# Optimization experiments

Measured on AMD Instinct MI355X. Metric: run time of the kernel, lower is better.

The kernel has to match this reference:

```python
import jax, jax.numpy as jnp
import numpy as np

D_MODEL = 128
D_INNER = 256
D_STATE = 16
D_CONV = 4
DT_RANK = 8
GROUPS = 4


def setup_inputs() -> dict:
    key = jax.random.key(0)
    ks = jax.random.split(key, 8)
    x = jax.random.normal(ks[0], (2, D_MODEL, 64, 64), dtype=jnp.float32)
    Win = jax.random.normal(ks[1], (2 * D_INNER, D_MODEL), dtype=jnp.float32) * (D_MODEL ** -0.5)
    conv_w = jax.random.normal(ks[2], (D_INNER, 1, D_CONV), dtype=jnp.float32) * 0.2
    conv_b = jnp.zeros((D_INNER,), dtype=jnp.float32)
    Wx = jax.random.normal(ks[3], (DT_RANK + 2 * D_STATE, D_INNER), dtype=jnp.float32) * (D_INNER ** -0.5)
    Wdt = jax.random.normal(ks[4], (D_INNER, DT_RANK), dtype=jnp.float32) * (DT_RANK ** -0.5)
    # bias chosen so softplus(bdt) ~ 0.01 (standard mamba dt init range)
    bdt = jnp.full((D_INNER,), -4.6, dtype=jnp.float32) + 0.1 * jax.random.normal(ks[5], (D_INNER,), dtype=jnp.float32)
    A_log = jnp.log(jnp.broadcast_to(jnp.arange(1, D_STATE + 1, dtype=jnp.float32), (D_INNER, D_STATE)))
    D = jnp.ones((D_INNER,), dtype=jnp.float32)
    Wout = jax.random.normal(ks[6], (D_MODEL, D_INNER), dtype=jnp.float32) * (D_INNER ** -0.5)
    gn_w = jnp.ones((D_MODEL,), dtype=jnp.float32)
    gn_b = jnp.zeros((D_MODEL,), dtype=jnp.float32)
    return {"x": x, "Win": Win, "conv_w": conv_w, "conv_b": conv_b, "Wx": Wx,
            "Wdt": Wdt, "bdt": bdt, "A_log": A_log, "D": D, "Wout": Wout,
            "gn_w": gn_w, "gn_b": gn_b}


def _mamba(xf, Win, conv_w, conv_b, Wx, Wdt, bdt, A_log, D, Wout):
    # xf: [1, L, d_model]
    d_inner = conv_w.shape[0]
    d_state = A_log.shape[1]
    xz = jnp.einsum('blc,ec->ble', xf, Win)                # [1, L, 2*di]
    u, z = jnp.split(xz, 2, axis=-1)
    # causal depthwise conv1d (pad left d_conv-1)
    uT = jnp.swapaxes(u, 1, 2)                             # [1, di, L]
    conv = jax.lax.conv_general_dilated(
        uT, conv_w, window_strides=(1,), padding=[(D_CONV - 1, 0)],
        feature_group_count=d_inner, dimension_numbers=('NCH', 'OIH', 'NCH'))
    u = jax.nn.silu(jnp.swapaxes(conv, 1, 2) + conv_b)      # [1, L, di]
    x_dbl = jnp.einsum('bld,ed->ble', u, Wx)
    dt = x_dbl[..., :DT_RANK]
    Bm = x_dbl[..., DT_RANK:DT_RANK + d_state]              # [1, L, n]
    Cm = x_dbl[..., DT_RANK + d_state:]                     # [1, L, n]
    delta = jax.nn.softplus(jnp.einsum('blr,dr->bld', dt, Wdt) + bdt)
    A = -jnp.exp(A_log)                                     # [di, n]
    dA = jnp.exp(jnp.einsum('bld,dn->bldn', delta, A))      # [1, L, di, n]
    dBu = jnp.einsum('bld,bln,bld->bldn', delta, Bm, u)     # [1, L, di, n]

    def step(h, inp):
        dA_l, dBu_l, C_l = inp
        h = dA_l * h + dBu_l                                # [1, di, n]
        y = jnp.einsum('bdn,bn->bd', h, C_l)
        return h, y

    h0 = jnp.zeros((1, d_inner, d_state), dtype=u.dtype)
    _, ys = jax.lax.scan(step, h0,
                         (jnp.swapaxes(dA, 0, 1), jnp.swapaxes(dBu, 0, 1), jnp.swapaxes(Cm, 0, 1)))
    y = jnp.swapaxes(ys, 0, 1)                              # [1, L, di]
    y = y + u * D
    y = y * jax.nn.silu(z)
    return jnp.einsum('bld,od->blo', y, Wout)


def reference(x, Win, conv_w, conv_b, Wx, Wdt, bdt, A_log, D, Wout, gn_w, gn_b):
    B, C, H, W = x.shape
    x_flat = jnp.transpose(x, (0, 2, 3, 1)).reshape(1, -1, C)   # [1, B*H*W, C]
    args = (Win, conv_w, conv_b, Wx, Wdt, bdt, A_log, D, Wout)
    y_fwd = _mamba(x_flat, *args)
    y_bwd = jnp.flip(_mamba(jnp.flip(x_flat, axis=1), *args), axis=1)
    x_recon = (y_fwd + y_bwd).reshape(B, H, W, C)
    x_recon = jnp.transpose(x_recon, (0, 3, 1, 2))              # [B, C, H, W]
    # GroupNorm(GROUPS, C) + SiLU
    xg = x_recon.reshape(B, GROUPS, C // GROUPS, H, W)
    mu = xg.mean(axis=(2, 3, 4), keepdims=True)
    var = xg.var(axis=(2, 3, 4), keepdims=True)
    xn = ((xg - mu) * jax.lax.rsqrt(var + 1e-5)).reshape(B, C, H, W)
    xn = xn * gn_w[:, None, None] + gn_b[:, None, None]
    return jax.nn.silu(xn) + x
```

## Files before the change

### kernel.cpp

```cpp
#include <hip/hip_runtime.h>
#include <math.h>

#define L_SEQ 8192
#define TCH 16
#define NCH 512

typedef short v8s __attribute__((ext_vector_type(8)));
typedef float v4f __attribute__((ext_vector_type(4)));

__device__ __forceinline__ float silu_f(float v) { return v / (1.f + expf(-v)); }

__device__ __forceinline__ unsigned short f2bf(float f) {
    unsigned u = __float_as_uint(f);
    u += 0x7fffu + ((u >> 16) & 1u);
    return (unsigned short)(u >> 16);
}
__device__ __forceinline__ float bf2f(unsigned short s) {
    return __uint_as_float(((unsigned)s) << 16);
}

__global__ __launch_bounds__(256) void k_xz_gemm(const float* __restrict__ x,
                                                 const float* __restrict__ Win,
                                                 const float* __restrict__ Wx,
                                                 const float* __restrict__ Wout,
                                                 float* __restrict__ ubuf,
                                                 float* __restrict__ zbuf,
                                                 unsigned short* __restrict__ Wx_bf,
                                                 unsigned short* __restrict__ Wout_bf) {
    if (blockIdx.y == 8) {
        int tid = blockIdx.x * 256 + threadIdx.x;
        if (tid < 10240) Wx_bf[tid] = f2bf(Wx[tid]);
        Wout_bf[tid] = f2bf(Wout[tid]);
        return;
    }
    __shared__ __align__(16) unsigned short As[64][136];
    __shared__ __align__(16) unsigned short Bs[64][136];
    int l0 = blockIdx.x * 64;
    int e0 = blockIdx.y * 64;
    int t = threadIdx.x;
    const float* xb = x + (l0 >> 12) * (128 * 4096) + (l0 & 4095);
    #pragma unroll
    for (int i = 0; i < 16; ++i) {
        int flat = t + 256 * i;
        int ll = flat & 63, cp = flat >> 6;
        float v0 = xb[(2 * cp) * 4096 + ll];
        float v1 = xb[(2 * cp + 1) * 4096 + ll];
        unsigned pk = (unsigned)f2bf(v0) | ((unsigned)f2bf(v1) << 16);
        *(unsigned*)&As[ll][2 * cp] = pk;
    }
    #pragma unroll
    for (int i = 0; i < 16; ++i) {
        int f = t + 256 * i;
        int row = f >> 6, cp = f & 63;
        float v0 = Win[(e0 + row) * 128 + 2 * cp];
        float v1 = Win[(e0 + row) * 128 + 2 * cp + 1];
        unsigned pk = (unsigned)f2bf(v0) | ((unsigned)f2bf(v1) << 16);
        *(unsigned*)&Bs[row][2 * cp] = pk;
    }
    __syncthreads();
    int lane = t & 63, wv = t >> 6;
    int quad = lane >> 4, l16 = lane & 15;
    v4f acc[4];
    #pragma unroll
    for (int nt = 0; nt < 4; ++nt) acc[nt] = (v4f){0.f, 0.f, 0.f, 0.f};
    #pragma unroll
    for (int k0 = 0; k0 < 128; k0 += 32) {
        v8s a = *(const v8s*)&As[wv * 16 + l16][k0 + quad * 8];
        #pragma unroll
        for (int nt = 0; nt < 4; ++nt) {
            v8s b = *(const v8s*)&Bs[nt * 16 + l16][k0 + quad * 8];
            acc[nt] = __builtin_amdgcn_mfma_f32_16x16x32_bf16(a, b, acc[nt], 0, 0, 0);
        }
    }
    #pragma unroll
    for (int nt = 0; nt < 4; ++nt) {
        int e = e0 + nt * 16 + l16;
        #pragma unroll
        for (int r = 0; r < 4; ++r) {
            int l = l0 + wv * 16 + quad * 4 + r;
            float v = acc[nt][r];
            if (e < 256) ubuf[l * 256 + e] = v;
            else         zbuf[l * 256 + e - 256] = v;
        }
    }
}

__global__ __launch_bounds__(256, 4) void k_pass1(const float* __restrict__ ubuf,
                                                  const unsigned short* __restrict__ Wx_bf,
                                                  const float* __restrict__ cw,
                                                  const float* __restrict__ cb,
                                                  const float* __restrict__ Wdt,
                                                  const float* __restrict__ bdt,
                                                  const float* __restrict__ Dp,
                                                  float* __restrict__ Cc,
                                                  float* __restrict__ cumSb,
                                                  unsigned short* __restrict__ ylb,
                                                  float* __restrict__ Sb,
                                                  unsigned short* __restrict__ Qb) {
    __shared__ __align__(16) unsigned short ucst[16][264];
    __shared__ __align__(16) unsigned short wxs[48][264];
    __shared__ float xs[16][48];
    int blk = blockIdx.x;
    int dir = blk >> 9, chunk = blk & 511;
    int m0 = chunk * TCH;
    int d = threadIdx.x;
    {
        const uint4* wxb = (const uint4*)Wx_bf;
        #pragma unroll
        for (int i = 0; i < 5; ++i) {
            int f = d + 256 * i;
            int row = f >> 5, col = (f & 31) * 8;
            *(uint4*)&wxs[row][col] = wxb[f];
        }
        uint4 z4 = {0u, 0u, 0u, 0u};
        int row = 40 + (d >> 5), col = (d & 31) * 8;
        *(uint4*)&wxs[row][col] = z4;
    }
    {
        float4 w4 = *(const float4*)&cw[d * 4];
        float cbd = cb[d];
        int m = m0 - 3;
        float p3 = (m >= 0) ? ubuf[(dir ? (8191 - m) : m) * 256 + d] : 0.f;
        m = m0 - 2;
        float p2 = (m >= 0) ? ubuf[(dir ? (8191 - m) : m) * 256 + d] : 0.f;
        m = m0 - 1;
        float p1 = (m >= 0) ? ubuf[(dir ? (8191 - m) : m) * 256 + d] : 0.f;
        #pragma unroll
        for (int i = 0; i < 16; ++i) {
            int mm = m0 + i;
            int l = dir ? (8191 - mm) : mm;
            float cur = ubuf[l * 256 + d];
            float v = cbd + w4.x * p3 + w4.y * p2 + w4.z * p1 + w4.w * cur;
            ucst[i][d] = f2bf(silu_f(v));
            p3 = p2; p2 = p1; p1 = cur;
        }
    }
    __syncthreads();
    {
        int lane = d & 63, wv = d >> 6;
        int quad = lane >> 4, l16 = lane & 15;
        if (wv < 3) {
            v4f acc = {0.f, 0.f, 0.f, 0.f};
            #pragma unroll
            for (int k0 = 0; k0 < 256; k0 += 32) {
                v8s a = *(const v8s*)&ucst[l16][k0 + quad * 8];
                v8s b = *(const v8s*)&wxs[wv * 16 + l16][k0 + quad * 8];
                acc = __builtin_amdgcn_mfma_f32_16x16x32_bf16(a, b, acc, 0, 0, 0);
            }
            #pragma unroll
            for (int r = 0; r < 4; ++r)
                xs[quad * 4 + r][wv * 16 + l16] = acc[r];
        }
    }
    __syncthreads();
    int gbase = dir * L_SEQ + m0;
    {
        int tl = d >> 4, n = d & 15;
        Cc[(gbase + tl) * 16 + n] = xs[tl][24 + n];
    }
    float wdt[8];
    *(float4*)&wdt[0] = *(const float4*)&Wdt[d * 8];
    *(float4*)&wdt[4] = *(const float4*)&Wdt[d * 8 + 4];
    float bd = bdt[d], Dd = Dp[d];
    float h[16];
    #pragma unroll
    for (int n = 0; n < 16; ++n) h[n] = 0.f;
    float cumS = 0.f;
    for (int tl = 0; tl < 16; ++tl) {
        float a = bd;
        #pragma unroll
        for (int r = 0; r < 8; ++r) a = fmaf(xs[tl][r], wdt[r], a);
        float dlt = (a > 20.f) ? a : log1pf(expf(a));
        cumS += dlt;
        float rr = expf(-dlt);
        float uq = bf2f(ucst[tl][d]);
        float p = dlt * uq;
        float am = 1.f, y = 0.f;
        #pragma unroll
        for (int n = 0; n < 16; ++n) {
            am *= rr;
            h[n] = fmaf(am, h[n], p * xs[tl][8 + n]);
            y = fmaf(h[n], xs[tl][24 + n], y);
        }
        int g = gbase + tl;
        cumSb[g * 256 + d] = cumS;
        ylb[g * 256 + d] = f2bf(fmaf(uq, Dd, y));
    }
    int cbk = dir * NCH + chunk;
    Sb[cbk * 256 + d] = cumS;
    #pragma unroll
    for (int n = 0; n < 16; ++n) Qb[(cbk * 16 + n) * 256 + d] = f2bf(h[n]);
}

__global__ __launch_bounds__(256, 4) void k_scan2(const float* __restrict__ Sb,
                                                  const unsigned short* __restrict__ Qb,
                                                  unsigned short* __restrict__ Hin) {
    __shared__ float Ag[8][32], Bg[8][32];
    int blk = blockIdx.x;
    int dir = blk >> 7;
    int rem = blk & 127;
    int n = rem >> 3, dg = rem & 7;
    int t = threadIdx.x;
    int cg = t >> 5, dl = t & 31;
    int d = dg * 32 + dl;
    float np1 = (float)(n + 1);
    int cbase = dir * NCH + cg * 64;
    float A = 1.f, B = 0.f;
    #pragma unroll 4
    for (int i = 0; i < 64; ++i) {
        int cbk = cbase + i;
        float a = expf(-Sb[cbk * 256 + d] * np1);
        float b = bf2f(Qb[(cbk * 16 + n) * 256 + d]);
        A = a * A;
        B = fmaf(a, B, b);
    }
    Ag[cg][dl] = A; Bg[cg][dl] = B;
    __syncthreads();
    float H = 0.f;
    for (int g = 0; g < cg; ++g) H = fmaf(Ag[g][dl], H, Bg[g][dl]);
    #pragma unroll 4
    for (int i = 0; i < 64; ++i) {
        int cbk = cbase + i;
        Hin[(cbk * 16 + n) * 256 + d] = f2bf(H);
        float a = expf(-Sb[cbk * 256 + d] * np1);
        float b = bf2f(Qb[(cbk * 16 + n) * 256 + d]);
        H = fmaf(a, H, b);
    }
}

__global__ __launch_bounds__(512) void k_yout(const float* __restrict__ cumSb,
                                              const unsigned short* __restrict__ ylb,
                                              const float* __restrict__ Cc,
                                              const unsigned short* __restrict__ Hin,
                                              const float* __restrict__ zbuf,
                                              const unsigned short* __restrict__ Wout_bf,
                                              float* __restrict__ outp,
                                              float* __restrict__ pbuf) {
    __shared__ __align__(16) unsigned short Ws[128][264];
    __shared__ __align__(16) unsigned short Ys[32][264];
    __shared__ float Cs[2][32][16];
    int blk = blockIdx.x;
    int l0 = blk * 32;
    int t = threadIdx.x;
    int d = t & 255, sub = t >> 8;
    {
        const uint4* wb = (const uint4*)Wout_bf;
        #pragma unroll
        for (int i = 0; i < 8; ++i) {
            int f = t + 512 * i;
            int row = f >> 5, col = (f & 31) * 8;
            *(uint4*)&Ws[row][col] = wb[f];
        }
    }
    #pragma unroll
    for (int j = 0; j < 2; ++j) {
        int flat = t + 512 * j;
        int dirx = flat >> 9, idx = flat & 511;
        int i = idx >> 4, n = idx & 15;
        int g = dirx ? (L_SEQ + 8191 - (l0 + i)) : (l0 + i);
        Cs[dirx][i][n] = Cc[g * 16 + n];
    }
    __syncthreads();
    {
        int lwin = l0 + 16 * sub;
        int cf = lwin >> 4;
        int cbw = 511 - cf;
        float Hf[16], Hb[16];
        #pragma unroll
        for (int n = 0; n < 16; ++n) {
            Hf[n] = bf2f(Hin[(cf * 16 + n) * 256 + d]);
            Hb[n] = bf2f(Hin[((NCH + cbw) * 16 + n) * 256 + d]);
        }
        for (int i = 0; i < 16; ++i) {
            int l = lwin + i;
            int li = l - l0;
            int gf = l, gb = L_SEQ + 8191 - l;
            float csf = cumSb[gf * 256 + d], ylf = bf2f(ylb[gf * 256 + d]);
            float csb = cumSb[gb * 256 + d], ylv = bf2f(ylb[gb * 256 + d]);
            float rf = expf(-csf), rb = expf(-csb);
            float af = 1.f, ab = 1.f, corr = 0.f;
            #pragma unroll
            for (int n = 0; n < 16; ++n) {
                af *= rf; ab *= rb;
                corr = fmaf(Cs[0][li][n] * af, Hf[n], corr);
                corr = fmaf(Cs[1][li][n] * ab, Hb[n], corr);
            }
            float y = ylf + ylv + corr;
            float z = zbuf[l * 256 + d];
            Ys[li][d] = f2bf(y * silu_f(z));
        }
    }
    __syncthreads();
    int lane = t & 63, wv = t >> 6;
    int quad = lane >> 4, l16 = lane & 15;
    v4f acc[2];
    acc[0] = (v4f){0.f, 0.f, 0.f, 0.f};
    acc[1] = (v4f){0.f, 0.f, 0.f, 0.f};
    #pragma unroll
    for (int k0 = 0; k0 < 256; k0 += 32) {
        v8s a = *(const v8s*)&Ws[wv * 16 + l16][k0 + quad * 8];
        #pragma unroll
        for (int nt = 0; nt < 2; ++nt) {
            v8s b = *(const v8s*)&Ys[nt * 16 + l16][k0 + quad * 8];
            acc[nt] = __builtin_amdgcn_mfma_f32_16x16x32_bf16(a, b, acc[nt], 0, 0, 0);
        }
    }
    float s1 = 0.f, s2 = 0.f;
    #pragma unroll
    for (int nt = 0; nt < 2; ++nt) {
        int l = l0 + nt * 16 + l16;
        #pragma unroll
        for (int r = 0; r < 4; ++r) {
            int c = wv * 16 + quad * 4 + r;
            float v = acc[nt][r];
            outp[c * L_SEQ + l] = v;
            s1 += v; s2 += v * v;
        }
    }
    __shared__ float r1[512], r2[512];
    r1[t] = s1; r2[t] = s2;
    __syncthreads();
    int seg = t >> 7, tl_ = t & 127;
    for (int s = 64; s > 0; s >>= 1) {
        if (tl_ < s) { r1[t] += r1[t + s]; r2[t] += r2[t + s]; }
        __syncthreads();
    }
    if (tl_ == 0) {
        pbuf[(blk * 4 + seg) * 2 + 0] = r1[t];
        pbuf[(blk * 4 + seg) * 2 + 1] = r2[t];
    }
}

__global__ __launch_bounds__(256) void k_gnred(const float* __restrict__ pbuf,
                                               float* __restrict__ gns) {
    __shared__ float red[16][16];
    int t = threadIdx.x;
    int o = t >> 4;
    int part = t & 15;
    int b = o >> 3, g = (o >> 1) & 3, s = o & 1;
    float acc = 0.f;
    #pragma unroll
    for (int k = 0; k < 8; ++k) {
        int bx = b * 128 + part * 8 + k;
        acc += pbuf[(bx * 4 + g) * 2 + s];
    }
    red[o][part] = acc;
    __syncthreads();
    if (part == 0) {
        float sum = 0.f;
        #pragma unroll
        for (int p = 0; p < 16; ++p) sum += red[o][p];
        gns[o] = sum;
    }
}

__global__ __launch_bounds__(256) void k_final(const float* __restrict__ outp,
                                               const float* __restrict__ gns,
                                               const float* __restrict__ gw,
                                               const float* __restrict__ gb,
                                               const float* __restrict__ x,
                                               float* __restrict__ out) {
    int idx = blockIdx.x * 256 + threadIdx.x;
    int c = idx >> 13;
    int l = idx & 8191;
    int b = l >> 12;
    int pos = l & 4095;
    int g = c >> 5;
    int bg = b * 4 + g;
    const float inv_n = 1.f / 131072.f;
    float mean = gns[bg * 2 + 0] * inv_n;
    float var = gns[bg * 2 + 1] * inv_n - mean * mean;
    float rstd = rsqrtf(var + 1e-5f);
    float v = outp[idx];
    float xn = (v - mean) * rstd * gw[c] + gb[c];
    int xi = b * (128 * 4096) + c * 4096 + pos;
    out[xi] = silu_f(xn) + x[xi];
}

extern "C" void kernel_launch(void* const* d_in, const int* in_sizes, int n_in,
                              void* d_out, int out_size, void* d_ws, size_t ws_size,
                              hipStream_t stream) {
    const float* x      = (const float*)d_in[0];
    const float* Win    = (const float*)d_in[1];
    const float* conv_w = (const float*)d_in[2];
    const float* conv_b = (const float*)d_in[3];
    const float* Wx     = (const float*)d_in[4];
    const float* Wdt    = (const float*)d_in[5];
    const float* bdt    = (const float*)d_in[6];
    const float* Dp     = (const float*)d_in[8];
    const float* Wout   = (const float*)d_in[9];
    const float* gn_w   = (const float*)d_in[10];
    const float* gn_b   = (const float*)d_in[11];
    float* out = (float*)d_out;
    float* ws  = (float*)d_ws;

    float* ubuf  = ws;
    float* zbuf  = ubuf  + 2097152;
    float* Cc    = zbuf  + 2097152;
    float* cumSb = Cc    + 262144;
    float* Sb    = cumSb + 4194304;
    float* outp  = Sb    + 262144;
    float* pbuf  = outp  + 1048576;
    float* gns   = pbuf  + 2048;
    unsigned short* ylb     = (unsigned short*)(gns + 16);
    unsigned short* Qb      = ylb + 4194304;
    unsigned short* Hin     = Qb + 4194304;
    unsigned short* Wx_bf   = Hin + 4194304;
    unsigned short* Wout_bf = Wx_bf + 10240;

    k_xz_gemm<<<dim3(128, 9), 256, 0, stream>>>(x, Win, Wx, Wout, ubuf, zbuf,
                                                Wx_bf, Wout_bf);
    k_pass1<<<1024, 256, 0, stream>>>(ubuf, Wx_bf, conv_w, conv_b, Wdt, bdt, Dp,
                                      Cc, cumSb, ylb, Sb, Qb);
    k_scan2<<<256, 256, 0, stream>>>(Sb, Qb, Hin);
    k_yout<<<256, 512, 0, stream>>>(cumSb, ylb, Cc, Hin, zbuf, Wout_bf,
                                    outp, pbuf);
    k_gnred<<<1, 256, 0, stream>>>(pbuf, gns);
    k_final<<<4096, 256, 0, stream>>>(outp, gns, gn_w, gn_b, x, out);
}
```

Before: 157.4 us.

## Fuse GroupNorm reduction via atomics, store decay products, widen scan and vectorize loads

Removes the separate GroupNorm reduction kernel: each k_yout wave reduces its partial sums with shuffles and adds them atomically into gns, which the first kernel zeroes. k_pass1 now stores the running product of exp(-dt) instead of the cumulative sum, so k_yout no longer computes exp on it. Shared-memory B/C rows are read with float4 vector loads. k_scan2 uses 1024 threads, each scanning 16 chunks instead of 64, giving more parallelism but a longer serial combine across 32 groups. k_yout loads the Wout fragments straight into registers instead of staging them in shared memory, and k_final processes four elements per thread with float4 accesses; the atomics make the sum order nondeterministic.

```diff
diff --git a/kernel.cpp b/kernel.cpp
--- a/kernel.cpp
+++ b/kernel.cpp
@@ -26,9 +26,11 @@
                                                  float* __restrict__ ubuf,
                                                  float* __restrict__ zbuf,
                                                  unsigned short* __restrict__ Wx_bf,
-                                                 unsigned short* __restrict__ Wout_bf) {
+                                                 unsigned short* __restrict__ Wout_bf,
+                                                 float* __restrict__ gns) {
     if (blockIdx.y == 8) {
         int tid = blockIdx.x * 256 + threadIdx.x;
+        if (tid < 16) gns[tid] = 0.f;
         if (tid < 10240) Wx_bf[tid] = f2bf(Wx[tid]);
         Wout_bf[tid] = f2bf(Wout[tid]);
         return;
@@ -93,13 +95,13 @@
                                                   const float* __restrict__ bdt,
                                                   const float* __restrict__ Dp,
                                                   float* __restrict__ Cc,
-                                                  float* __restrict__ cumSb,
+                                                  float* __restrict__ rbuf,
                                                   unsigned short* __restrict__ ylb,
                                                   float* __restrict__ Sb,
                                                   unsigned short* __restrict__ Qb) {
     __shared__ __align__(16) unsigned short ucst[16][264];
     __shared__ __align__(16) unsigned short wxs[48][264];
-    __shared__ float xs[16][48];
+    __shared__ __align__(16) float xs[16][48];
     int blk = blockIdx.x;
     int dir = blk >> 9, chunk = blk & 511;
     int m0 = chunk * TCH;
@@ -165,25 +167,39 @@
     float h[16];
     #pragma unroll
     for (int n = 0; n < 16; ++n) h[n] = 0.f;
-    float cumS = 0.f;
+    float cumS = 0.f, rcum = 1.f;
     for (int tl = 0; tl < 16; ++tl) {
+        const float4* xr = (const float4*)&xs[tl][0];
+        float dv[8];
+        *(float4*)&dv[0] = xr[0];
+        *(float4*)&dv[4] = xr[1];
         float a = bd;
         #pragma unroll
-        for (int r = 0; r < 8; ++r) a = fmaf(xs[tl][r], wdt[r], a);
+        for (int r = 0; r < 8; ++r) a = fmaf(dv[r], wdt[r], a);
         float dlt = (a > 20.f) ? a : log1pf(expf(a));
         cumS += dlt;
         float rr = expf(-dlt);
+        rcum *= rr;
         float uq = bf2f(ucst[tl][d]);
         float p = dlt * uq;
+        float Bv[16], Cv[16];
+        *(float4*)&Bv[0]  = xr[2];
+        *(float4*)&Bv[4]  = xr[3];
+        *(float4*)&Bv[8]  = xr[4];
+        *(float4*)&Bv[12] = xr[5];
+        *(float4*)&Cv[0]  = xr[6];
+        *(float4*)&Cv[4]  = xr[7];
+        *(float4*)&Cv[8]  = xr[8];
+        *(float4*)&Cv[12] = xr[9];
         float am = 1.f, y = 0.f;
         #pragma unroll
         for (int n = 0; n < 16; ++n) {
             am *= rr;
-            h[n] = fmaf(am, h[n], p * xs[tl][8 + n]);
-            y = fmaf(h[n], xs[tl][24 + n], y);
+            h[n] = fmaf(am, h[n], p * Bv[n]);
+            y = fmaf(h[n], Cv[n], y);
         }
         int g = gbase + tl;
-        cumSb[g * 256 + d] = cumS;
+        rbuf[g * 256 + d] = rcum;
         ylb[g * 256 + d] = f2bf(fmaf(uq, Dd, y));
     }
     int cbk = dir * NCH + chunk;
@@ -192,10 +208,10 @@
     for (int n = 0; n < 16; ++n) Qb[(cbk * 16 + n) * 256 + d] = f2bf(h[n]);
 }
 
-__global__ __launch_bounds__(256, 4) void k_scan2(const float* __restrict__ Sb,
-                                                  const unsigned short* __restrict__ Qb,
-                                                  unsigned short* __restrict__ Hin) {
-    __shared__ float Ag[8][32], Bg[8][32];
+__global__ __launch_bounds__(1024, 4) void k_scan2(const float* __restrict__ Sb,
+                                                   const unsigned short* __restrict__ Qb,
+                                                   unsigned short* __restrict__ Hin) {
+    __shared__ float Ag[32][32], Bg[32][32];
     int blk = blockIdx.x;
     int dir = blk >> 7;
     int rem = blk & 127;
@@ -204,10 +220,10 @@
     int cg = t >> 5, dl = t & 31;
     int d = dg * 32 + dl;
     float np1 = (float)(n + 1);
-    int cbase = dir * NCH + cg * 64;
+    int cbase = dir * NCH + cg * 16;
     float A = 1.f, B = 0.f;
     #pragma unroll 4
-    for (int i = 0; i < 64; ++i) {
+    for (int i = 0; i < 16; ++i) {
         int cbk = cbase + i;
         float a = expf(-Sb[cbk * 256 + d] * np1);
         float b = bf2f(Qb[(cbk * 16 + n) * 256 + d]);
@@ -219,7 +235,7 @@
     float H = 0.f;
     for (int g = 0; g < cg; ++g) H = fmaf(Ag[g][dl], H, Bg[g][dl]);
     #pragma unroll 4
-    for (int i = 0; i < 64; ++i) {
+    for (int i = 0; i < 16; ++i) {
         int cbk = cbase + i;
         Hin[(cbk * 16 + n) * 256 + d] = f2bf(H);
         float a = expf(-Sb[cbk * 256 + d] * np1);
@@ -228,30 +244,20 @@
     }
 }
 
-__global__ __launch_bounds__(512) void k_yout(const float* __restrict__ cumSb,
-                                              const unsigned short* __restrict__ ylb,
-                                              const float* __restrict__ Cc,
-                                              const unsigned short* __restrict__ Hin,
-                                              const float* __restrict__ zbuf,
-                                              const unsigned short* __restrict__ Wout_bf,
-                                              float* __restrict__ outp,
-                                              float* __restrict__ pbuf) {
-    __shared__ __align__(16) unsigned short Ws[128][264];
+__global__ __launch_bounds__(512, 4) void k_yout(const float* __restrict__ rbuf,
+                                                 const unsigned short* __restrict__ ylb,
+                                                 const float* __restrict__ Cc,
+                                                 const unsigned short* __restrict__ Hin,
+                                                 const float* __restrict__ zbuf,
+                                                 const unsigned short* __restrict__ Wout_bf,
+                                                 float* __restrict__ outp,
+                                                 float* __restrict__ gns) {
     __shared__ __align__(16) unsigned short Ys[32][264];
-    __shared__ float Cs[2][32][16];
+    __shared__ __align__(16) float Cs[2][32][16];
     int blk = blockIdx.x;
     int l0 = blk * 32;
     int t = threadIdx.x;
     int d = t & 255, sub = t >> 8;
-    {
-        const uint4* wb = (const uint4*)Wout_bf;
-        #pragma unroll
-        for (int i = 0; i < 8; ++i) {
-            int f = t + 512 * i;
-            int row = f >> 5, col = (f & 31) * 8;
-            *(uint4*)&Ws[row][col] = wb[f];
-        }
-    }
     #pragma unroll
     for (int j = 0; j < 2; ++j) {
         int flat = t + 512 * j;
@@ -275,15 +281,23 @@
             int l = lwin + i;
             int li = l - l0;
             int gf = l, gb = L_SEQ + 8191 - l;
-            float csf = cumSb[gf * 256 + d], ylf = bf2f(ylb[gf * 256 + d]);
-            float csb = cumSb[gb * 256 + d], ylv = bf2f(ylb[gb * 256 + d]);
-            float rf = expf(-csf), rb = expf(-csb);
+            float rf = rbuf[gf * 256 + d], ylf = bf2f(ylb[gf * 256 + d]);
+            float rb = rbuf[gb * 256 + d], ylv = bf2f(ylb[gb * 256 + d]);
+            float C0v[16], C1v[16];
+            *(float4*)&C0v[0]  = *(const float4*)&Cs[0][li][0];
+            *(float4*)&C0v[4]  = *(const float4*)&Cs[0][li][4];
+            *(float4*)&C0v[8]  = *(const float4*)&Cs[0][li][8];
+            *(float4*)&C0v[12] = *(const float4*)&Cs[0][li][12];
+            *(float4*)&C1v[0]  = *(const float4*)&Cs[1][li][0];
+            *(float4*)&C1v[4]  = *(const float4*)&Cs[1][li][4];
+            *(float4*)&C1v[8]  = *(const float4*)&Cs[1][li][8];
+            *(float4*)&C1v[12] = *(const float4*)&Cs[1][li][12];
             float af = 1.f, ab = 1.f, corr = 0.f;
             #pragma unroll
             for (int n = 0; n < 16; ++n) {
                 af *= rf; ab *= rb;
-                corr = fmaf(Cs[0][li][n] * af, Hf[n], corr);
-                corr = fmaf(Cs[1][li][n] * ab, Hb[n], corr);
+                corr = fmaf(C0v[n] * af, Hf[n], corr);
+                corr = fmaf(C1v[n] * ab, Hb[n], corr);
             }
             float y = ylf + ylv + corr;
             float z = zbuf[l * 256 + d];
@@ -293,16 +307,20 @@
     __syncthreads();
     int lane = t & 63, wv = t >> 6;
     int quad = lane >> 4, l16 = lane & 15;
+    const unsigned short* wr = Wout_bf + (wv * 16 + l16) * 256 + quad * 8;
+    v8s wfrag[8];
+    #pragma unroll
+    for (int j = 0; j < 8; ++j) wfrag[j] = *(const v8s*)&wr[32 * j];
     v4f acc[2];
     acc[0] = (v4f){0.f, 0.f, 0.f, 0.f};
     acc[1] = (v4f){0.f, 0.f, 0.f, 0.f};
     #pragma unroll
-    for (int k0 = 0; k0 < 256; k0 += 32) {
-        v8s a = *(const v8s*)&Ws[wv * 16 + l16][k0 + quad * 8];
+    for (int j = 0; j < 8; ++j) {
+        int k0 = 32 * j;
         #pragma unroll
         for (int nt = 0; nt < 2; ++nt) {
             v8s b = *(const v8s*)&Ys[nt * 16 + l16][k0 + quad * 8];
-            acc[nt] = __builtin_amdgcn_mfma_f32_16x16x32_bf16(a, b, acc[nt], 0, 0, 0);
+            acc[nt] = __builtin_amdgcn_mfma_f32_16x16x32_bf16(wfrag[j], b, acc[nt], 0, 0, 0);
         }
     }
     float s1 = 0.f, s2 = 0.f;
@@ -317,40 +335,15 @@
             s1 += v; s2 += v * v;
         }
     }
-    __shared__ float r1[512], r2[512];
-    r1[t] = s1; r2[t] = s2;
-    __syncthreads();
-    int seg = t >> 7, tl_ = t & 127;
-    for (int s = 64; s > 0; s >>= 1) {
-        if (tl_ < s) { r1[t] += r1[t + s]; r2[t] += r2[t + s]; }
-        __syncthreads();
-    }
-    if (tl_ == 0) {
-        pbuf[(blk * 4 + seg) * 2 + 0] = r1[t];
-        pbuf[(blk * 4 + seg) * 2 + 1] = r2[t];
-    }
-}
-
-__global__ __launch_bounds__(256) void k_gnred(const float* __restrict__ pbuf,
-                                               float* __restrict__ gns) {
-    __shared__ float red[16][16];
-    int t = threadIdx.x;
-    int o = t >> 4;
-    int part = t & 15;
-    int b = o >> 3, g = (o >> 1) & 3, s = o & 1;
-    float acc = 0.f;
-    #pragma unroll
-    for (int k = 0; k < 8; ++k) {
-        int bx = b * 128 + part * 8 + k;
-        acc += pbuf[(bx * 4 + g) * 2 + s];
-    }
-    red[o][part] = acc;
-    __syncthreads();
-    if (part == 0) {
-        float sum = 0.f;
-        #pragma unroll
-        for (int p = 0; p < 16; ++p) sum += red[o][p];
-        gns[o] = sum;
+    #pragma unroll
+    for (int off = 32; off > 0; off >>= 1) {
+        s1 += __shfl_xor(s1, off);
+        s2 += __shfl_xor(s2, off);
+    }
+    if (lane == 0) {
+        int bg = (l0 >> 12) * 4 + (wv >> 1);
+        atomicAdd(&gns[bg * 2 + 0], s1);
+        atomicAdd(&gns[bg * 2 + 1], s2);
     }
 }
 
@@ -360,21 +353,27 @@
                                                const float* __restrict__ gb,
                                                const float* __restrict__ x,
                                                float* __restrict__ out) {
-    int idx = blockIdx.x * 256 + threadIdx.x;
+    int idx4 = blockIdx.x * 256 + threadIdx.x;
+    int idx = idx4 << 2;
     int c = idx >> 13;
     int l = idx & 8191;
     int b = l >> 12;
     int pos = l & 4095;
-    int g = c >> 5;
-    int bg = b * 4 + g;
+    int bg = b * 4 + (c >> 5);
     const float inv_n = 1.f / 131072.f;
     float mean = gns[bg * 2 + 0] * inv_n;
     float var = gns[bg * 2 + 1] * inv_n - mean * mean;
     float rstd = rsqrtf(var + 1e-5f);
-    float v = outp[idx];
-    float xn = (v - mean) * rstd * gw[c] + gb[c];
+    float gwc = gw[c], gbc = gb[c];
+    float4 v = *(const float4*)&outp[idx];
     int xi = b * (128 * 4096) + c * 4096 + pos;
-    out[xi] = silu_f(xn) + x[xi];
+    float4 xr = *(const float4*)&x[xi];
+    float4 o;
+    o.x = silu_f((v.x - mean) * rstd * gwc + gbc) + xr.x;
+    o.y = silu_f((v.y - mean) * rstd * gwc + gbc) + xr.y;
+    o.z = silu_f((v.z - mean) * rstd * gwc + gbc) + xr.z;
+    o.w = silu_f((v.w - mean) * rstd * gwc + gbc) + xr.w;
+    *(float4*)&out[xi] = o;
 }
 
 extern "C" void kernel_launch(void* const* d_in, const int* in_sizes, int n_in,
@@ -397,24 +396,22 @@
     float* ubuf  = ws;
     float* zbuf  = ubuf  + 2097152;
     float* Cc    = zbuf  + 2097152;
-    float* cumSb = Cc    + 262144;
-    float* Sb    = cumSb + 4194304;
+    float* rbuf  = Cc    + 262144;
+    float* Sb    = rbuf  + 4194304;
     float* outp  = Sb    + 262144;
-    float* pbuf  = outp  + 1048576;
-    float* gns   = pbuf  + 2048;
-    unsigned short* ylb     = (unsigned short*)(gns + 16);
+    float* gns   = outp  + 1048576;
+    unsigned short* ylb     = (unsigned short*)(gns + 2048);
     unsigned short* Qb      = ylb + 4194304;
     unsigned short* Hin     = Qb + 4194304;
     unsigned short* Wx_bf   = Hin + 4194304;
     unsigned short* Wout_bf = Wx_bf + 10240;
 
     k_xz_gemm<<<dim3(128, 9), 256, 0, stream>>>(x, Win, Wx, Wout, ubuf, zbuf,
-                                                Wx_bf, Wout_bf);
+                                                Wx_bf, Wout_bf, gns);
     k_pass1<<<1024, 256, 0, stream>>>(ubuf, Wx_bf, conv_w, conv_b, Wdt, bdt, Dp,
-                                      Cc, cumSb, ylb, Sb, Qb);
-    k_scan2<<<256, 256, 0, stream>>>(Sb, Qb, Hin);
-    k_yout<<<256, 512, 0, stream>>>(cumSb, ylb, Cc, Hin, zbuf, Wout_bf,
-                                    outp, pbuf);
-    k_gnred<<<1, 256, 0, stream>>>(pbuf, gns);
-    k_final<<<4096, 256, 0, stream>>>(outp, gns, gn_w, gn_b, x, out);
-}
+                                      Cc, rbuf, ylb, Sb, Qb);
+    k_scan2<<<256, 1024, 0, stream>>>(Sb, Qb, Hin);
+    k_yout<<<256, 512, 0, stream>>>(rbuf, ylb, Cc, Hin, zbuf, Wout_bf,
+                                    outp, gns);
+    k_final<<<1024, 256, 0, stream>>>(outp, gns, gn_w, gn_b, x, out);
+}
```

After: 210.5 us. +33.7%, slower.
